# Kernel tuning notes

Measured on AMD Instinct MI355X. Metric: run time of the kernel, lower is better.

## Reference

```python
import jax, jax.numpy as jnp
import numpy as np

B, T, D_MODEL, HEAD = 4, 4096, 1024, 64

def setup_inputs() -> dict:
    key = jax.random.key(0)
    ks = jax.random.split(key, 7)
    s = 0.02  # typical init scale
    return {
        "x":  jax.random.normal(ks[0], (B, T, D_MODEL), dtype=jnp.float32),
        "Wq": jax.random.normal(ks[1], (D_MODEL, HEAD), dtype=jnp.float32) * s,
        "bq": jnp.zeros((HEAD,), dtype=jnp.float32),
        "Wk": jax.random.normal(ks[2], (D_MODEL, HEAD), dtype=jnp.float32) * s,
        "bk": jnp.zeros((HEAD,), dtype=jnp.float32),
        "Wv": jax.random.normal(ks[3], (D_MODEL, HEAD), dtype=jnp.float32) * s,
        "bv": jnp.zeros((HEAD,), dtype=jnp.float32),
    }

def reference(x, Wq, bq, Wk, bk, Wv, bv):
    Bz, Tz, C = x.shape
    q = x @ Wq + bq                      # (B,T,H)
    k = x @ Wk + bk                      # (B,T,H)
    v = x @ Wv + bv                      # (B,T,H)
    # NOTE: original scales by sqrt(C) = sqrt(d_model), not sqrt(head_size)
    att = jnp.einsum("bth,bsh->bts", q, k) / jnp.sqrt(jnp.float32(C))
    causal = jnp.tril(jnp.ones((Tz, Tz), dtype=bool))
    att = jnp.where(causal, att, -jnp.inf)
    att = jax.nn.softmax(att, axis=-1)
    return jnp.einsum("bts,bsh->bth", att, v)  # (B,T,H)
```

## Files before the change

kernel.cpp:

```cpp
#include <hip/hip_runtime.h>
#include <hip/hip_bf16.h>
#include <hip/hip_fp16.h>

#define T_SEQ 4096
#define DMODEL 1024
#define HEAD 64
#define NBATCH 4
#define NSEG 576
#define S2LOG 0.04508422f

typedef __attribute__((ext_vector_type(8))) short bf16x8;
typedef __attribute__((ext_vector_type(4))) float f32x4;

__device__ __forceinline__ unsigned short f2bf(float f) {
    unsigned int b = __float_as_uint(f);
    unsigned int r = b + 0x7FFFu + ((b >> 16) & 1u);
    return (unsigned short)(r >> 16);
}
__device__ __forceinline__ unsigned int pk_bf16(float a, float b) {
    __hip_bfloat162 h = __float22bfloat162_rn(make_float2(a, b));
    unsigned int u; __builtin_memcpy(&u, &h, 4); return u;
}

__global__ __launch_bounds__(256) void prep_w(
    const float* __restrict__ Wq, const float* __restrict__ Wk,
    const float* __restrict__ Wv, unsigned short* __restrict__ Wtb)
{
    __shared__ unsigned short tl[64 * 72];
    const int bid = blockIdx.x;
    const int m   = bid >> 4;
    const int k0  = (bid & 15) * 64;
    const float* W = (m == 0) ? Wq : (m == 1) ? Wk : Wv;
    const int t  = threadIdx.x;
    const int kr = t >> 2, qtr = t & 3;
#pragma unroll
    for (int i = 0; i < 4; ++i) {
        float4 wv4 = *(const float4*)&W[(k0 + kr) * 64 + qtr * 16 + i * 4];
        tl[(qtr * 16 + i * 4 + 0) * 72 + kr] = f2bf(wv4.x);
        tl[(qtr * 16 + i * 4 + 1) * 72 + kr] = f2bf(wv4.y);
        tl[(qtr * 16 + i * 4 + 2) * 72 + kr] = f2bf(wv4.z);
        tl[(qtr * 16 + i * 4 + 3) * 72 + kr] = f2bf(wv4.w);
    }
    __syncthreads();
#pragma unroll
    for (int c = 0; c < 2; ++c) {
        const int lin = c * 256 + t;
        const int n = lin >> 3, k8 = lin & 7;
        *(uint4*)&Wtb[((long)(m * 64 + n)) * 1024 + k0 + k8 * 8] =
            *(const uint4*)&tl[n * 72 + k8 * 8];
    }
}

__global__ __launch_bounds__(256, 2) void qkv_mfma(
    const float* __restrict__ x, const unsigned short* __restrict__ Wtb,
    const float* __restrict__ bq, const float* __restrict__ bk,
    const float* __restrict__ bv,
    unsigned short* __restrict__ qo, unsigned short* __restrict__ ko,
    unsigned short* __restrict__ vt)
{
    __shared__ __align__(16) unsigned short x_s[2][32 * 136];
    const int t    = threadIdx.x;
    const int lane = t & 63;
    const int l15  = lane & 15, quad = lane >> 4;
    const int w    = __builtin_amdgcn_readfirstlane(t >> 6);
    const long row0 = (long)blockIdx.x * 32;

    float bias[3];
#pragma unroll
    for (int ntl = 0; ntl < 3; ++ntl) {
        const int c = w * 48 + ntl * 16 + l15;
        bias[ntl] = (c < 64) ? bq[c] : (c < 128) ? bk[c - 64] : bv[c - 128];
    }
    f32x4 acc[2][3];
#pragma unroll
    for (int mt = 0; mt < 2; ++mt)
#pragma unroll
        for (int ntl = 0; ntl < 3; ++ntl)
            acc[mt][ntl] = (f32x4){bias[ntl], bias[ntl], bias[ntl], bias[ntl]};

    const int srow = t >> 3, sseg = t & 7;
    const float* xp = x + (row0 + srow) * DMODEL + sseg * 16;

    float4 xv[4];
#pragma unroll
    for (int i = 0; i < 4; ++i) xv[i] = *(const float4*)(xp + i * 4);
    {
        unsigned int pk_[8];
#pragma unroll
        for (int i = 0; i < 4; ++i) {
            pk_[i * 2]     = pk_bf16(xv[i].x, xv[i].y);
            pk_[i * 2 + 1] = pk_bf16(xv[i].z, xv[i].w);
        }
        *(uint4*)&x_s[0][srow * 136 + sseg * 16]     = *(const uint4*)&pk_[0];
        *(uint4*)&x_s[0][srow * 136 + sseg * 16 + 8] = *(const uint4*)&pk_[4];
    }
    __syncthreads();

    for (int sg = 0; sg < 8; ++sg) {
        if (sg + 1 < 8)
#pragma unroll
            for (int i = 0; i < 4; ++i)
                xv[i] = *(const float4*)(xp + (sg + 1) * 128 + i * 4);
        bf16x8 wf[3][4];
#pragma unroll
        for (int ntl = 0; ntl < 3; ++ntl)
#pragma unroll
            for (int kq = 0; kq < 4; ++kq)
                wf[ntl][kq] = *(const bf16x8*)&Wtb[((long)(w * 48 + ntl * 16 + l15)) * 1024
                                                   + sg * 128 + kq * 32 + quad * 8];
#pragma unroll
        for (int mt = 0; mt < 2; ++mt)
#pragma unroll
            for (int kq = 0; kq < 4; ++kq) {
                bf16x8 a = *(const bf16x8*)&x_s[sg & 1][(mt * 16 + l15) * 136 + kq * 32 + quad * 8];
#pragma unroll
                for (int ntl = 0; ntl < 3; ++ntl)
                    acc[mt][ntl] = __builtin_amdgcn_mfma_f32_16x16x32_bf16(a, wf[ntl][kq], acc[mt][ntl], 0, 0, 0);
            }
        if (sg + 1 < 8) {
            unsigned int pk_[8];
#pragma unroll
            for (int i = 0; i < 4; ++i) {
                pk_[i * 2]     = pk_bf16(xv[i].x, xv[i].y);
                pk_[i * 2 + 1] = pk_bf16(xv[i].z, xv[i].w);
            }
            *(uint4*)&x_s[(sg + 1) & 1][srow * 136 + sseg * 16]     = *(const uint4*)&pk_[0];
            *(uint4*)&x_s[(sg + 1) & 1][srow * 136 + sseg * 16 + 8] = *(const uint4*)&pk_[4];
        }
        __syncthreads();
    }
#pragma unroll
    for (int mt = 0; mt < 2; ++mt)
#pragma unroll
        for (int ntl = 0; ntl < 3; ++ntl) {
            const int c = w * 48 + ntl * 16 + l15;
            const long tr0 = row0 + mt * 16 + quad * 4;
            if (c < 64) {
#pragma unroll
                for (int r = 0; r < 4; ++r)
                    qo[(tr0 + r) * HEAD + c] = f2bf(acc[mt][ntl][r] * S2LOG);
            } else if (c < 128) {
#pragma unroll
                for (int r = 0; r < 4; ++r)
                    ko[(tr0 + r) * HEAD + (c - 64)] = f2bf(acc[mt][ntl][r]);
            } else {
                const int b = (int)(tr0 >> 12), tloc = (int)(tr0 & 4095);
                uint2 pv;
                pv.x = pk_bf16(acc[mt][ntl][0], acc[mt][ntl][1]);
                pv.y = pk_bf16(acc[mt][ntl][2], acc[mt][ntl][3]);
                *(uint2*)&vt[((long)(b * HEAD + (c - 128))) * T_SEQ + tloc] = pv;
            }
        }
}

__global__ __launch_bounds__(256, 3) void flash_seg(
    const unsigned short* __restrict__ qg,
    const unsigned short* __restrict__ kg,
    const unsigned short* __restrict__ vtg,
    __half* __restrict__ opart, float* __restrict__ ml)
{
    __shared__ __align__(16) unsigned short p_s[4][32 * 72];
    const int t0   = threadIdx.x;
    const int lane = t0 & 63;
    const int l15  = lane & 15, quad = lane >> 4;
    const int wv   = __builtin_amdgcn_readfirstlane(t0 >> 6);

    const int sid = (NSEG - 1) - (int)blockIdx.x;
    int kk = 0, pref = 0;
#pragma unroll
    for (int i = 0; i < 7; ++i) {
        const int cnt = 16 * (kk + 1);
        if (sid >= pref + cnt) { pref += cnt; ++kk; }
    }
    const int S   = kk + 1;
    const int rem = sid - pref;
    const int t   = kk * 16 + rem / S;
    const int si  = rem % S;
    const int r0  = t * 32;
    const int nck = (t + 2) >> 1;
    const int c0  = (si * nck) / S, c1 = ((si + 1) * nck) / S;
    const int b   = wv;
    const long bbase = (long)b * T_SEQ;
    const int gidx = b * NSEG + sid;

    bf16x8 qf[2][2];
#pragma unroll
    for (int s = 0; s < 2; ++s)
#pragma unroll
        for (int h = 0; h < 2; ++h)
            qf[s][h] = *(const bf16x8*)&qg[(bbase + r0 + s * 16 + l15) * HEAD + h * 32 + quad * 8];

    f32x4 o[2][4];
#pragma unroll
    for (int s = 0; s < 2; ++s)
#pragma unroll
        for (int dt = 0; dt < 4; ++dt) o[s][dt] = (f32x4){0.f, 0.f, 0.f, 0.f};
    float mrun[2] = {-30000.f, -30000.f}, lrun[2] = {0.f, 0.f};

    unsigned short* ps = p_s[wv];

    for (int c = c0; c < c1; ++c) {
        const int key0 = c * 64;
        bf16x8 kf[4][2];
#pragma unroll
        for (int mt = 0; mt < 4; ++mt) {
            int krow = key0 + mt * 16 + l15; if (krow > T_SEQ - 1) krow = T_SEQ - 1;
            const unsigned short* kp = &kg[(bbase + krow) * HEAD + quad * 8];
            kf[mt][0] = *(const bf16x8*)kp;
            kf[mt][1] = *(const bf16x8*)(kp + 32);
        }
        f32x4 st[2][4];
#pragma unroll
        for (int s = 0; s < 2; ++s)
#pragma unroll
            for (int mt = 0; mt < 4; ++mt) {
                f32x4 z = (f32x4){0.f, 0.f, 0.f, 0.f};
                z = __builtin_amdgcn_mfma_f32_16x16x32_bf16(kf[mt][0], qf[s][0], z, 0, 0, 0);
                st[s][mt] = __builtin_amdgcn_mfma_f32_16x16x32_bf16(kf[mt][1], qf[s][1], z, 0, 0, 0);
            }
        bf16x8 vf[4][2];
#pragma unroll
        for (int dt = 0; dt < 4; ++dt)
#pragma unroll
            for (int g = 0; g < 2; ++g) {
                int kof = key0 + g * 32 + quad * 8; if (kof > T_SEQ - 8) kof = T_SEQ - 8;
                vf[dt][g] = *(const bf16x8*)&vtg[((long)(b * HEAD + dt * 16 + l15)) * T_SEQ + kof];
            }
        if (key0 + 63 > r0) {
#pragma unroll
            for (int s = 0; s < 2; ++s) {
                const int row = r0 + s * 16 + l15;
#pragma unroll
                for (int mt = 0; mt < 4; ++mt)
#pragma unroll
                    for (int r = 0; r < 4; ++r) {
                        const int key = key0 + mt * 16 + quad * 4 + r;
                        st[s][mt][r] = (key <= row) ? st[s][mt][r] : -30000.f;
                    }
            }
        }
#pragma unroll
        for (int s = 0; s < 2; ++s) {
            float mx = st[s][0][0];
#pragma unroll
            for (int mt = 0; mt < 4; ++mt)
#pragma unroll
                for (int r = 0; r < 4; ++r) mx = fmaxf(mx, st[s][mt][r]);
            mx = fmaxf(mx, __shfl_xor(mx, 16));
            mx = fmaxf(mx, __shfl_xor(mx, 32));
            const float mn = fmaxf(mrun[s], mx);
            const float al = exp2f(mrun[s] - mn);
            mrun[s] = mn;
            float psum = 0.f;
#pragma unroll
            for (int mt = 0; mt < 4; ++mt) {
                float e0 = exp2f(st[s][mt][0] - mn), e1 = exp2f(st[s][mt][1] - mn);
                float e2 = exp2f(st[s][mt][2] - mn), e3 = exp2f(st[s][mt][3] - mn);
                psum += (e0 + e1) + (e2 + e3);
                *(unsigned int*)&ps[(s * 16 + l15) * 72 + mt * 16 + quad * 4]     = pk_bf16(e0, e1);
                *(unsigned int*)&ps[(s * 16 + l15) * 72 + mt * 16 + quad * 4 + 2] = pk_bf16(e2, e3);
            }
            psum += __shfl_xor(psum, 16);
            psum += __shfl_xor(psum, 32);
            lrun[s] = lrun[s] * al + psum;
#pragma unroll
            for (int dt = 0; dt < 4; ++dt)
#pragma unroll
                for (int r = 0; r < 4; ++r) o[s][dt][r] *= al;
        }
        __builtin_amdgcn_wave_barrier();
        bf16x8 pf[2][2];
#pragma unroll
        for (int s = 0; s < 2; ++s)
#pragma unroll
            for (int g = 0; g < 2; ++g)
                pf[s][g] = *(const bf16x8*)&ps[(s * 16 + l15) * 72 + g * 32 + quad * 8];
        __builtin_amdgcn_wave_barrier();
#pragma unroll
        for (int s = 0; s < 2; ++s)
#pragma unroll
            for (int dt = 0; dt < 4; ++dt) {
                o[s][dt] = __builtin_amdgcn_mfma_f32_16x16x32_bf16(vf[dt][0], pf[s][0], o[s][dt], 0, 0, 0);
                o[s][dt] = __builtin_amdgcn_mfma_f32_16x16x32_bf16(vf[dt][1], pf[s][1], o[s][dt], 0, 0, 0);
            }
    }
    __half* op = opart + (long)gidx * 2048;
#pragma unroll
    for (int s = 0; s < 2; ++s) {
#pragma unroll
        for (int dt = 0; dt < 4; ++dt) {
            __half2 h0 = __floats2half2_rn(o[s][dt][0], o[s][dt][1]);
            __half2 h1 = __floats2half2_rn(o[s][dt][2], o[s][dt][3]);
            uint2 u; __builtin_memcpy(&u.x, &h0, 4); __builtin_memcpy(&u.y, &h1, 4);
            *(uint2*)&op[(s * 16 + l15) * HEAD + dt * 16 + quad * 4] = u;
        }
        if (quad == 0) {
            ml[(long)gidx * 64 + s * 16 + l15]      = mrun[s];
            ml[(long)gidx * 64 + 32 + s * 16 + l15] = lrun[s];
        }
    }
}

__global__ __launch_bounds__(256) void merge_seg(
    const __half* __restrict__ opart, const float* __restrict__ ml,
    float* __restrict__ out)
{
    const int bid = blockIdx.x;
    const int t = bid & 127, b = bid >> 7;
    const int kk = t >> 4, S = kk + 1;
    const int base_sid = 8 * kk * (kk + 1) + (t & 15) * S;
    const int tid = threadIdx.x;
    const int row = tid >> 3, col0 = (tid & 7) * 8;

    float m[8], l[8], M = -30000.f;
    for (int si = 0; si < S; ++si) {
        const long g = (long)(b * NSEG + base_sid + si);
        m[si] = ml[g * 64 + row];
        l[si] = ml[g * 64 + 32 + row];
        M = fmaxf(M, m[si]);
    }
    float acc[8];
#pragma unroll
    for (int j = 0; j < 8; ++j) acc[j] = 0.f;
    float L = 0.f;
    for (int si = 0; si < S; ++si) {
        const float wgt = exp2f(m[si] - M);
        L += wgt * l[si];
        const __half* op = opart + (long)(b * NSEG + base_sid + si) * 2048 + row * 64 + col0;
        uint4 u = *(const uint4*)op;
        __half2 h01, h23, h45, h67;
        __builtin_memcpy(&h01, &u.x, 4); __builtin_memcpy(&h23, &u.y, 4);
        __builtin_memcpy(&h45, &u.z, 4); __builtin_memcpy(&h67, &u.w, 4);
        float2 f01 = __half22float2(h01), f23 = __half22float2(h23);
        float2 f45 = __half22float2(h45), f67 = __half22float2(h67);
        acc[0] += wgt * f01.x; acc[1] += wgt * f01.y;
        acc[2] += wgt * f23.x; acc[3] += wgt * f23.y;
        acc[4] += wgt * f45.x; acc[5] += wgt * f45.y;
        acc[6] += wgt * f67.x; acc[7] += wgt * f67.y;
    }
    const float inv = 1.f / L;
    float4 o0 = {acc[0] * inv, acc[1] * inv, acc[2] * inv, acc[3] * inv};
    float4 o1 = {acc[4] * inv, acc[5] * inv, acc[6] * inv, acc[7] * inv};
    float* dst = out + ((long)(b * T_SEQ + t * 32 + row)) * HEAD + col0;
    *(float4*)dst = o0;
    *(float4*)(dst + 4) = o1;
}

extern "C" void kernel_launch(void* const* d_in, const int* in_sizes, int n_in,
                              void* d_out, int out_size, void* d_ws, size_t ws_size,
                              hipStream_t stream) {
    const float* x  = (const float*)d_in[0];
    const float* Wq = (const float*)d_in[1];
    const float* bq = (const float*)d_in[2];
    const float* Wk = (const float*)d_in[3];
    const float* bk = (const float*)d_in[4];
    const float* Wv = (const float*)d_in[5];
    const float* bv = (const float*)d_in[6];
    float* outp = (float*)d_out;

    char* wsb = (char*)d_ws;
    unsigned short* wtb = (unsigned short*)(wsb);
    unsigned short* qw  = (unsigned short*)(wsb + 393216);
    unsigned short* kw  = (unsigned short*)(wsb + 2490368);
    unsigned short* vtw = (unsigned short*)(wsb + 4587520);
    __half* opart       = (__half*)(wsb + 6684672);
    float*  mlp         = (float*)(wsb + 16121856);

    prep_w<<<dim3(48), dim3(256), 0, stream>>>(Wq, Wk, Wv, wtb);
    qkv_mfma<<<dim3(512), dim3(256), 0, stream>>>(
        x, wtb, bq, bk, bv, qw, kw, vtw);
    flash_seg<<<dim3(NSEG), dim3(256), 0, stream>>>(qw, kw, vtw, opart, mlp);
    merge_seg<<<dim3(512), dim3(256), 0, stream>>>(opart, mlp, outp);
}
```

Before: 177.3 us.

## Prefetch K/V double-buffered, split flash blocks per batch, drop LDS staging in QKV

The flash kernel now runs one wave per block, with the batch taken from the block index, and launches four times as many blocks. It double-buffers K and V fragments in registers so the next chunk's loads are issued before the current chunk is processed. The QKV projection kernel drops its shared-memory staging and barriers: each lane reads fp32 x directly from global memory in MFMA fragment layout and converts it to bf16 in registers. The aim is to hide global-load latency and remove barrier overhead, at the cost of more registers and less coalesced x loads.

```diff
diff --git a/kernel.cpp b/kernel.cpp
--- a/kernel.cpp
+++ b/kernel.cpp
@@ -58,7 +58,6 @@
     unsigned short* __restrict__ qo, unsigned short* __restrict__ ko,
     unsigned short* __restrict__ vt)
 {
-    __shared__ __align__(16) unsigned short x_s[2][32 * 136];
     const int t    = threadIdx.x;
     const int lane = t & 63;
     const int l15  = lane & 15, quad = lane >> 4;
@@ -78,56 +77,41 @@
         for (int ntl = 0; ntl < 3; ++ntl)
             acc[mt][ntl] = (f32x4){bias[ntl], bias[ntl], bias[ntl], bias[ntl]};
 
-    const int srow = t >> 3, sseg = t & 7;
-    const float* xp = x + (row0 + srow) * DMODEL + sseg * 16;
-
-    float4 xv[4];
-#pragma unroll
-    for (int i = 0; i < 4; ++i) xv[i] = *(const float4*)(xp + i * 4);
-    {
-        unsigned int pk_[8];
-#pragma unroll
-        for (int i = 0; i < 4; ++i) {
-            pk_[i * 2]     = pk_bf16(xv[i].x, xv[i].y);
-            pk_[i * 2 + 1] = pk_bf16(xv[i].z, xv[i].w);
-        }
-        *(uint4*)&x_s[0][srow * 136 + sseg * 16]     = *(const uint4*)&pk_[0];
-        *(uint4*)&x_s[0][srow * 136 + sseg * 16 + 8] = *(const uint4*)&pk_[4];
-    }
-    __syncthreads();
-
+    const float* xa0 = x + (row0 + l15) * DMODEL + quad * 8;
+    const float* xa1 = x + (row0 + 16 + l15) * DMODEL + quad * 8;
+    const unsigned short* wb = Wtb + ((long)(w * 48 + l15)) * DMODEL + quad * 8;
+
+#pragma unroll 2
     for (int sg = 0; sg < 8; ++sg) {
-        if (sg + 1 < 8)
-#pragma unroll
-            for (int i = 0; i < 4; ++i)
-                xv[i] = *(const float4*)(xp + (sg + 1) * 128 + i * 4);
+        float4 xr[2][4][2];
+#pragma unroll
+        for (int kq = 0; kq < 4; ++kq) {
+            xr[0][kq][0] = *(const float4*)(xa0 + sg * 128 + kq * 32);
+            xr[0][kq][1] = *(const float4*)(xa0 + sg * 128 + kq * 32 + 4);
+            xr[1][kq][0] = *(const float4*)(xa1 + sg * 128 + kq * 32);
+            xr[1][kq][1] = *(const float4*)(xa1 + sg * 128 + kq * 32 + 4);
+        }
         bf16x8 wf[3][4];
 #pragma unroll
         for (int ntl = 0; ntl < 3; ++ntl)
 #pragma unroll
             for (int kq = 0; kq < 4; ++kq)
-                wf[ntl][kq] = *(const bf16x8*)&Wtb[((long)(w * 48 + ntl * 16 + l15)) * 1024
-                                                   + sg * 128 + kq * 32 + quad * 8];
+                wf[ntl][kq] = *(const bf16x8*)(wb + (long)ntl * 16 * DMODEL
+                                               + sg * 128 + kq * 32);
 #pragma unroll
         for (int mt = 0; mt < 2; ++mt)
 #pragma unroll
             for (int kq = 0; kq < 4; ++kq) {
-                bf16x8 a = *(const bf16x8*)&x_s[sg & 1][(mt * 16 + l15) * 136 + kq * 32 + quad * 8];
+                unsigned int u[4];
+                u[0] = pk_bf16(xr[mt][kq][0].x, xr[mt][kq][0].y);
+                u[1] = pk_bf16(xr[mt][kq][0].z, xr[mt][kq][0].w);
+                u[2] = pk_bf16(xr[mt][kq][1].x, xr[mt][kq][1].y);
+                u[3] = pk_bf16(xr[mt][kq][1].z, xr[mt][kq][1].w);
+                bf16x8 a; __builtin_memcpy(&a, u, 16);
 #pragma unroll
                 for (int ntl = 0; ntl < 3; ++ntl)
                     acc[mt][ntl] = __builtin_amdgcn_mfma_f32_16x16x32_bf16(a, wf[ntl][kq], acc[mt][ntl], 0, 0, 0);
             }
-        if (sg + 1 < 8) {
-            unsigned int pk_[8];
-#pragma unroll
-            for (int i = 0; i < 4; ++i) {
-                pk_[i * 2]     = pk_bf16(xv[i].x, xv[i].y);
-                pk_[i * 2 + 1] = pk_bf16(xv[i].z, xv[i].w);
-            }
-            *(uint4*)&x_s[(sg + 1) & 1][srow * 136 + sseg * 16]     = *(const uint4*)&pk_[0];
-            *(uint4*)&x_s[(sg + 1) & 1][srow * 136 + sseg * 16 + 8] = *(const uint4*)&pk_[4];
-        }
-        __syncthreads();
     }
 #pragma unroll
     for (int mt = 0; mt < 2; ++mt)
@@ -153,19 +137,115 @@
         }
 }
 
-__global__ __launch_bounds__(256, 3) void flash_seg(
+struct KV { bf16x8 kf[4][2]; bf16x8 vf[4][2]; };
+
+__device__ __forceinline__ void load_kv(
+    const unsigned short* __restrict__ kg, const unsigned short* __restrict__ vtg,
+    long bbase, int b, int key0, int l15, int quad, KV& r)
+{
+#pragma unroll
+    for (int mt = 0; mt < 4; ++mt) {
+        int krow = key0 + mt * 16 + l15; if (krow > T_SEQ - 1) krow = T_SEQ - 1;
+        const unsigned short* kp = &kg[(bbase + krow) * HEAD + quad * 8];
+        r.kf[mt][0] = *(const bf16x8*)kp;
+        r.kf[mt][1] = *(const bf16x8*)(kp + 32);
+    }
+#pragma unroll
+    for (int dt = 0; dt < 4; ++dt)
+#pragma unroll
+        for (int g = 0; g < 2; ++g) {
+            int kof = key0 + g * 32 + quad * 8; if (kof > T_SEQ - 8) kof = T_SEQ - 8;
+            r.vf[dt][g] = *(const bf16x8*)&vtg[((long)(b * HEAD + dt * 16 + l15)) * T_SEQ + kof];
+        }
+}
+
+__device__ __forceinline__ void process_chunk(
+    int key0, int r0, int l15, int quad,
+    const bf16x8 (&qf)[2][2], const KV& kv, unsigned short* ps,
+    f32x4 (&o)[2][4], float (&mrun)[2], float (&lrun)[2])
+{
+    f32x4 st[2][4];
+#pragma unroll
+    for (int s = 0; s < 2; ++s)
+#pragma unroll
+        for (int mt = 0; mt < 4; ++mt) {
+            f32x4 z = (f32x4){0.f, 0.f, 0.f, 0.f};
+            z = __builtin_amdgcn_mfma_f32_16x16x32_bf16(kv.kf[mt][0], qf[s][0], z, 0, 0, 0);
+            st[s][mt] = __builtin_amdgcn_mfma_f32_16x16x32_bf16(kv.kf[mt][1], qf[s][1], z, 0, 0, 0);
+        }
+    if (key0 + 63 > r0) {
+#pragma unroll
+        for (int s = 0; s < 2; ++s) {
+            const int row = r0 + s * 16 + l15;
+#pragma unroll
+            for (int mt = 0; mt < 4; ++mt)
+#pragma unroll
+                for (int r = 0; r < 4; ++r) {
+                    const int key = key0 + mt * 16 + quad * 4 + r;
+                    st[s][mt][r] = (key <= row) ? st[s][mt][r] : -30000.f;
+                }
+        }
+    }
+#pragma unroll
+    for (int s = 0; s < 2; ++s) {
+        float mx = st[s][0][0];
+#pragma unroll
+        for (int mt = 0; mt < 4; ++mt)
+#pragma unroll
+            for (int r = 0; r < 4; ++r) mx = fmaxf(mx, st[s][mt][r]);
+        mx = fmaxf(mx, __shfl_xor(mx, 16));
+        mx = fmaxf(mx, __shfl_xor(mx, 32));
+        const float mn = fmaxf(mrun[s], mx);
+        const float al = exp2f(mrun[s] - mn);
+        mrun[s] = mn;
+        float psum = 0.f;
+#pragma unroll
+        for (int mt = 0; mt < 4; ++mt) {
+            float e0 = exp2f(st[s][mt][0] - mn), e1 = exp2f(st[s][mt][1] - mn);
+            float e2 = exp2f(st[s][mt][2] - mn), e3 = exp2f(st[s][mt][3] - mn);
+            psum += (e0 + e1) + (e2 + e3);
+            *(unsigned int*)&ps[(s * 16 + l15) * 72 + mt * 16 + quad * 4]     = pk_bf16(e0, e1);
+            *(unsigned int*)&ps[(s * 16 + l15) * 72 + mt * 16 + quad * 4 + 2] = pk_bf16(e2, e3);
+        }
+        psum += __shfl_xor(psum, 16);
+        psum += __shfl_xor(psum, 32);
+        lrun[s] = lrun[s] * al + psum;
+#pragma unroll
+        for (int dt = 0; dt < 4; ++dt)
+#pragma unroll
+            for (int r = 0; r < 4; ++r) o[s][dt][r] *= al;
+    }
+    __builtin_amdgcn_wave_barrier();
+    bf16x8 pf[2][2];
+#pragma unroll
+    for (int s = 0; s < 2; ++s)
+#pragma unroll
+        for (int g = 0; g < 2; ++g)
+            pf[s][g] = *(const bf16x8*)&ps[(s * 16 + l15) * 72 + g * 32 + quad * 8];
+    __builtin_amdgcn_wave_barrier();
+#pragma unroll
+    for (int s = 0; s < 2; ++s)
+#pragma unroll
+        for (int dt = 0; dt < 4; ++dt) {
+            o[s][dt] = __builtin_amdgcn_mfma_f32_16x16x32_bf16(kv.vf[dt][0], pf[s][0], o[s][dt], 0, 0, 0);
+            o[s][dt] = __builtin_amdgcn_mfma_f32_16x16x32_bf16(kv.vf[dt][1], pf[s][1], o[s][dt], 0, 0, 0);
+        }
+}
+
+__global__ __launch_bounds__(64, 2) void flash_seg(
     const unsigned short* __restrict__ qg,
     const unsigned short* __restrict__ kg,
     const unsigned short* __restrict__ vtg,
     __half* __restrict__ opart, float* __restrict__ ml)
 {
-    __shared__ __align__(16) unsigned short p_s[4][32 * 72];
-    const int t0   = threadIdx.x;
-    const int lane = t0 & 63;
+    __shared__ __align__(16) unsigned short p_s[32 * 72];
+    const int lane = threadIdx.x & 63;
     const int l15  = lane & 15, quad = lane >> 4;
-    const int wv   = __builtin_amdgcn_readfirstlane(t0 >> 6);
-
-    const int sid = (NSEG - 1) - (int)blockIdx.x;
+
+    const int bid = (int)blockIdx.x;
+    const int sid = (NSEG - 1) - (bid >> 2);
+    const int b   = bid & 3;
+
     int kk = 0, pref = 0;
 #pragma unroll
     for (int i = 0; i < 7; ++i) {
@@ -179,7 +259,6 @@
     const int r0  = t * 32;
     const int nck = (t + 2) >> 1;
     const int c0  = (si * nck) / S, c1 = ((si + 1) * nck) / S;
-    const int b   = wv;
     const long bbase = (long)b * T_SEQ;
     const int gidx = b * NSEG + sid;
 
@@ -197,93 +276,18 @@
         for (int dt = 0; dt < 4; ++dt) o[s][dt] = (f32x4){0.f, 0.f, 0.f, 0.f};
     float mrun[2] = {-30000.f, -30000.f}, lrun[2] = {0.f, 0.f};
 
-    unsigned short* ps = p_s[wv];
-
+    KV A, B;
+    load_kv(kg, vtg, bbase, b, c0 * 64, l15, quad, A);
     for (int c = c0; c < c1; ++c) {
-        const int key0 = c * 64;
-        bf16x8 kf[4][2];
-#pragma unroll
-        for (int mt = 0; mt < 4; ++mt) {
-            int krow = key0 + mt * 16 + l15; if (krow > T_SEQ - 1) krow = T_SEQ - 1;
-            const unsigned short* kp = &kg[(bbase + krow) * HEAD + quad * 8];
-            kf[mt][0] = *(const bf16x8*)kp;
-            kf[mt][1] = *(const bf16x8*)(kp + 32);
-        }
-        f32x4 st[2][4];
-#pragma unroll
-        for (int s = 0; s < 2; ++s)
-#pragma unroll
-            for (int mt = 0; mt < 4; ++mt) {
-                f32x4 z = (f32x4){0.f, 0.f, 0.f, 0.f};
-                z = __builtin_amdgcn_mfma_f32_16x16x32_bf16(kf[mt][0], qf[s][0], z, 0, 0, 0);
-                st[s][mt] = __builtin_amdgcn_mfma_f32_16x16x32_bf16(kf[mt][1], qf[s][1], z, 0, 0, 0);
-            }
-        bf16x8 vf[4][2];
-#pragma unroll
-        for (int dt = 0; dt < 4; ++dt)
-#pragma unroll
-            for (int g = 0; g < 2; ++g) {
-                int kof = key0 + g * 32 + quad * 8; if (kof > T_SEQ - 8) kof = T_SEQ - 8;
-                vf[dt][g] = *(const bf16x8*)&vtg[((long)(b * HEAD + dt * 16 + l15)) * T_SEQ + kof];
-            }
-        if (key0 + 63 > r0) {
-#pragma unroll
-            for (int s = 0; s < 2; ++s) {
-                const int row = r0 + s * 16 + l15;
-#pragma unroll
-                for (int mt = 0; mt < 4; ++mt)
-#pragma unroll
-                    for (int r = 0; r < 4; ++r) {
-                        const int key = key0 + mt * 16 + quad * 4 + r;
-                        st[s][mt][r] = (key <= row) ? st[s][mt][r] : -30000.f;
-                    }
-            }
-        }
-#pragma unroll
-        for (int s = 0; s < 2; ++s) {
-            float mx = st[s][0][0];
-#pragma unroll
-            for (int mt = 0; mt < 4; ++mt)
-#pragma unroll
-                for (int r = 0; r < 4; ++r) mx = fmaxf(mx, st[s][mt][r]);
-            mx = fmaxf(mx, __shfl_xor(mx, 16));
-            mx = fmaxf(mx, __shfl_xor(mx, 32));
-            const float mn = fmaxf(mrun[s], mx);
-            const float al = exp2f(mrun[s] - mn);
-            mrun[s] = mn;
-            float psum = 0.f;
-#pragma unroll
-            for (int mt = 0; mt < 4; ++mt) {
-                float e0 = exp2f(st[s][mt][0] - mn), e1 = exp2f(st[s][mt][1] - mn);
-                float e2 = exp2f(st[s][mt][2] - mn), e3 = exp2f(st[s][mt][3] - mn);
-                psum += (e0 + e1) + (e2 + e3);
-                *(unsigned int*)&ps[(s * 16 + l15) * 72 + mt * 16 + quad * 4]     = pk_bf16(e0, e1);
-                *(unsigned int*)&ps[(s * 16 + l15) * 72 + mt * 16 + quad * 4 + 2] = pk_bf16(e2, e3);
-            }
-            psum += __shfl_xor(psum, 16);
-            psum += __shfl_xor(psum, 32);
-            lrun[s] = lrun[s] * al + psum;
-#pragma unroll
-            for (int dt = 0; dt < 4; ++dt)
-#pragma unroll
-                for (int r = 0; r < 4; ++r) o[s][dt][r] *= al;
-        }
-        __builtin_amdgcn_wave_barrier();
-        bf16x8 pf[2][2];
-#pragma unroll
-        for (int s = 0; s < 2; ++s)
-#pragma unroll
-            for (int g = 0; g < 2; ++g)
-                pf[s][g] = *(const bf16x8*)&ps[(s * 16 + l15) * 72 + g * 32 + quad * 8];
-        __builtin_amdgcn_wave_barrier();
-#pragma unroll
-        for (int s = 0; s < 2; ++s)
-#pragma unroll
-            for (int dt = 0; dt < 4; ++dt) {
-                o[s][dt] = __builtin_amdgcn_mfma_f32_16x16x32_bf16(vf[dt][0], pf[s][0], o[s][dt], 0, 0, 0);
-                o[s][dt] = __builtin_amdgcn_mfma_f32_16x16x32_bf16(vf[dt][1], pf[s][1], o[s][dt], 0, 0, 0);
-            }
-    }
+        if (((c - c0) & 1) == 0) {
+            if (c + 1 < c1) load_kv(kg, vtg, bbase, b, (c + 1) * 64, l15, quad, B);
+            process_chunk(c * 64, r0, l15, quad, qf, A, p_s, o, mrun, lrun);
+        } else {
+            if (c + 1 < c1) load_kv(kg, vtg, bbase, b, (c + 1) * 64, l15, quad, A);
+            process_chunk(c * 64, r0, l15, quad, qf, B, p_s, o, mrun, lrun);
+        }
+    }
+
     __half* op = opart + (long)gidx * 2048;
 #pragma unroll
     for (int s = 0; s < 2; ++s) {
@@ -369,6 +373,6 @@
     prep_w<<<dim3(48), dim3(256), 0, stream>>>(Wq, Wk, Wv, wtb);
     qkv_mfma<<<dim3(512), dim3(256), 0, stream>>>(
         x, wtb, bq, bk, bv, qw, kw, vtw);
-    flash_seg<<<dim3(NSEG), dim3(256), 0, stream>>>(qw, kw, vtw, opart, mlp);
+    flash_seg<<<dim3(NSEG * NBATCH), dim3(64), 0, stream>>>(qw, kw, vtw, opart, mlp);
     merge_seg<<<dim3(512), dim3(256), 0, stream>>>(opart, mlp, outp);
 }
```

Measured after the change: 261.4 us. 47.4% more time.

## Halve QKV row tile and rebalance flash key-split segments for more blocks

Applied to the files above, without the earlier changes.

The QKV projection kernel now handles 16 rows per block instead of 32 and launches 1024 blocks, giving more parallelism but loading the weight fragments twice as often. The flash attention split-K schedule is redefined so each group of 8 query tiles gets an increasing number of key segments (up to 16), raising segment count from 576 to 1088 for better load balance. The merge kernel and workspace offsets are updated to match. The key/value row clamping is also removed, which saves address math and is safe only if reads never run past the sequence.

```diff
diff --git a/kernel.cpp b/kernel.cpp
--- a/kernel.cpp
+++ b/kernel.cpp
@@ -6,7 +6,7 @@
 #define DMODEL 1024
 #define HEAD 64
 #define NBATCH 4
-#define NSEG 576
+#define NSEG 1088
 #define S2LOG 0.04508422f
 
 typedef __attribute__((ext_vector_type(8))) short bf16x8;
@@ -58,12 +58,12 @@
     unsigned short* __restrict__ qo, unsigned short* __restrict__ ko,
     unsigned short* __restrict__ vt)
 {
-    __shared__ __align__(16) unsigned short x_s[2][32 * 136];
+    __shared__ __align__(16) unsigned short x_s[2][16 * 136];
     const int t    = threadIdx.x;
     const int lane = t & 63;
     const int l15  = lane & 15, quad = lane >> 4;
     const int w    = __builtin_amdgcn_readfirstlane(t >> 6);
-    const long row0 = (long)blockIdx.x * 32;
+    const long row0 = (long)blockIdx.x * 16;
 
     float bias[3];
 #pragma unroll
@@ -71,36 +71,30 @@
         const int c = w * 48 + ntl * 16 + l15;
         bias[ntl] = (c < 64) ? bq[c] : (c < 128) ? bk[c - 64] : bv[c - 128];
     }
-    f32x4 acc[2][3];
-#pragma unroll
-    for (int mt = 0; mt < 2; ++mt)
-#pragma unroll
-        for (int ntl = 0; ntl < 3; ++ntl)
-            acc[mt][ntl] = (f32x4){bias[ntl], bias[ntl], bias[ntl], bias[ntl]};
-
-    const int srow = t >> 3, sseg = t & 7;
-    const float* xp = x + (row0 + srow) * DMODEL + sseg * 16;
-
-    float4 xv[4];
-#pragma unroll
-    for (int i = 0; i < 4; ++i) xv[i] = *(const float4*)(xp + i * 4);
+    f32x4 acc[3];
+#pragma unroll
+    for (int ntl = 0; ntl < 3; ++ntl)
+        acc[ntl] = (f32x4){bias[ntl], bias[ntl], bias[ntl], bias[ntl]};
+
+    const int srow = t >> 4, sseg = t & 15;
+    const float* xp = x + (row0 + srow) * DMODEL + sseg * 8;
+
+    float4 xv[2];
+    xv[0] = *(const float4*)(xp);
+    xv[1] = *(const float4*)(xp + 4);
     {
-        unsigned int pk_[8];
-#pragma unroll
-        for (int i = 0; i < 4; ++i) {
-            pk_[i * 2]     = pk_bf16(xv[i].x, xv[i].y);
-            pk_[i * 2 + 1] = pk_bf16(xv[i].z, xv[i].w);
-        }
-        *(uint4*)&x_s[0][srow * 136 + sseg * 16]     = *(const uint4*)&pk_[0];
-        *(uint4*)&x_s[0][srow * 136 + sseg * 16 + 8] = *(const uint4*)&pk_[4];
+        unsigned int pk_[4];
+        pk_[0] = pk_bf16(xv[0].x, xv[0].y); pk_[1] = pk_bf16(xv[0].z, xv[0].w);
+        pk_[2] = pk_bf16(xv[1].x, xv[1].y); pk_[3] = pk_bf16(xv[1].z, xv[1].w);
+        *(uint4*)&x_s[0][srow * 136 + sseg * 8] = *(const uint4*)&pk_[0];
     }
     __syncthreads();
 
     for (int sg = 0; sg < 8; ++sg) {
-        if (sg + 1 < 8)
-#pragma unroll
-            for (int i = 0; i < 4; ++i)
-                xv[i] = *(const float4*)(xp + (sg + 1) * 128 + i * 4);
+        if (sg + 1 < 8) {
+            xv[0] = *(const float4*)(xp + (sg + 1) * 128);
+            xv[1] = *(const float4*)(xp + (sg + 1) * 128 + 4);
+        }
         bf16x8 wf[3][4];
 #pragma unroll
         for (int ntl = 0; ntl < 3; ++ntl)
@@ -109,48 +103,40 @@
                 wf[ntl][kq] = *(const bf16x8*)&Wtb[((long)(w * 48 + ntl * 16 + l15)) * 1024
                                                    + sg * 128 + kq * 32 + quad * 8];
 #pragma unroll
-        for (int mt = 0; mt < 2; ++mt)
-#pragma unroll
-            for (int kq = 0; kq < 4; ++kq) {
-                bf16x8 a = *(const bf16x8*)&x_s[sg & 1][(mt * 16 + l15) * 136 + kq * 32 + quad * 8];
-#pragma unroll
-                for (int ntl = 0; ntl < 3; ++ntl)
-                    acc[mt][ntl] = __builtin_amdgcn_mfma_f32_16x16x32_bf16(a, wf[ntl][kq], acc[mt][ntl], 0, 0, 0);
-            }
+        for (int kq = 0; kq < 4; ++kq) {
+            bf16x8 a = *(const bf16x8*)&x_s[sg & 1][l15 * 136 + kq * 32 + quad * 8];
+#pragma unroll
+            for (int ntl = 0; ntl < 3; ++ntl)
+                acc[ntl] = __builtin_amdgcn_mfma_f32_16x16x32_bf16(a, wf[ntl][kq], acc[ntl], 0, 0, 0);
+        }
         if (sg + 1 < 8) {
-            unsigned int pk_[8];
-#pragma unroll
-            for (int i = 0; i < 4; ++i) {
-                pk_[i * 2]     = pk_bf16(xv[i].x, xv[i].y);
-                pk_[i * 2 + 1] = pk_bf16(xv[i].z, xv[i].w);
-            }
-            *(uint4*)&x_s[(sg + 1) & 1][srow * 136 + sseg * 16]     = *(const uint4*)&pk_[0];
-            *(uint4*)&x_s[(sg + 1) & 1][srow * 136 + sseg * 16 + 8] = *(const uint4*)&pk_[4];
+            unsigned int pk_[4];
+            pk_[0] = pk_bf16(xv[0].x, xv[0].y); pk_[1] = pk_bf16(xv[0].z, xv[0].w);
+            pk_[2] = pk_bf16(xv[1].x, xv[1].y); pk_[3] = pk_bf16(xv[1].z, xv[1].w);
+            *(uint4*)&x_s[(sg + 1) & 1][srow * 136 + sseg * 8] = *(const uint4*)&pk_[0];
         }
         __syncthreads();
     }
 #pragma unroll
-    for (int mt = 0; mt < 2; ++mt)
-#pragma unroll
-        for (int ntl = 0; ntl < 3; ++ntl) {
-            const int c = w * 48 + ntl * 16 + l15;
-            const long tr0 = row0 + mt * 16 + quad * 4;
-            if (c < 64) {
-#pragma unroll
-                for (int r = 0; r < 4; ++r)
-                    qo[(tr0 + r) * HEAD + c] = f2bf(acc[mt][ntl][r] * S2LOG);
-            } else if (c < 128) {
-#pragma unroll
-                for (int r = 0; r < 4; ++r)
-                    ko[(tr0 + r) * HEAD + (c - 64)] = f2bf(acc[mt][ntl][r]);
-            } else {
-                const int b = (int)(tr0 >> 12), tloc = (int)(tr0 & 4095);
-                uint2 pv;
-                pv.x = pk_bf16(acc[mt][ntl][0], acc[mt][ntl][1]);
-                pv.y = pk_bf16(acc[mt][ntl][2], acc[mt][ntl][3]);
-                *(uint2*)&vt[((long)(b * HEAD + (c - 128))) * T_SEQ + tloc] = pv;
-            }
-        }
+    for (int ntl = 0; ntl < 3; ++ntl) {
+        const int c = w * 48 + ntl * 16 + l15;
+        const long tr0 = row0 + quad * 4;
+        if (c < 64) {
+#pragma unroll
+            for (int r = 0; r < 4; ++r)
+                qo[(tr0 + r) * HEAD + c] = f2bf(acc[ntl][r] * S2LOG);
+        } else if (c < 128) {
+#pragma unroll
+            for (int r = 0; r < 4; ++r)
+                ko[(tr0 + r) * HEAD + (c - 64)] = f2bf(acc[ntl][r]);
+        } else {
+            const int b = (int)(tr0 >> 12), tloc = (int)(tr0 & 4095);
+            uint2 pv;
+            pv.x = pk_bf16(acc[ntl][0], acc[ntl][1]);
+            pv.y = pk_bf16(acc[ntl][2], acc[ntl][3]);
+            *(uint2*)&vt[((long)(b * HEAD + (c - 128))) * T_SEQ + tloc] = pv;
+        }
+    }
 }
 
 __global__ __launch_bounds__(256, 3) void flash_seg(
@@ -168,13 +154,13 @@
     const int sid = (NSEG - 1) - (int)blockIdx.x;
     int kk = 0, pref = 0;
 #pragma unroll
-    for (int i = 0; i < 7; ++i) {
-        const int cnt = 16 * (kk + 1);
+    for (int i = 0; i < 15; ++i) {
+        const int cnt = 8 * (kk + 1);
         if (sid >= pref + cnt) { pref += cnt; ++kk; }
     }
     const int S   = kk + 1;
     const int rem = sid - pref;
-    const int t   = kk * 16 + rem / S;
+    const int t   = kk * 8 + rem / S;
     const int si  = rem % S;
     const int r0  = t * 32;
     const int nck = (t + 2) >> 1;
@@ -204,8 +190,7 @@
         bf16x8 kf[4][2];
 #pragma unroll
         for (int mt = 0; mt < 4; ++mt) {
-            int krow = key0 + mt * 16 + l15; if (krow > T_SEQ - 1) krow = T_SEQ - 1;
-            const unsigned short* kp = &kg[(bbase + krow) * HEAD + quad * 8];
+            const unsigned short* kp = &kg[(bbase + key0 + mt * 16 + l15) * HEAD + quad * 8];
             kf[mt][0] = *(const bf16x8*)kp;
             kf[mt][1] = *(const bf16x8*)(kp + 32);
         }
@@ -222,10 +207,9 @@
 #pragma unroll
         for (int dt = 0; dt < 4; ++dt)
 #pragma unroll
-            for (int g = 0; g < 2; ++g) {
-                int kof = key0 + g * 32 + quad * 8; if (kof > T_SEQ - 8) kof = T_SEQ - 8;
-                vf[dt][g] = *(const bf16x8*)&vtg[((long)(b * HEAD + dt * 16 + l15)) * T_SEQ + kof];
-            }
+            for (int g = 0; g < 2; ++g)
+                vf[dt][g] = *(const bf16x8*)&vtg[((long)(b * HEAD + dt * 16 + l15)) * T_SEQ
+                                                 + key0 + g * 32 + quad * 8];
         if (key0 + 63 > r0) {
 #pragma unroll
             for (int s = 0; s < 2; ++s) {
@@ -284,6 +268,7 @@
                 o[s][dt] = __builtin_amdgcn_mfma_f32_16x16x32_bf16(vf[dt][1], pf[s][1], o[s][dt], 0, 0, 0);
             }
     }
+
     __half* op = opart + (long)gidx * 2048;
 #pragma unroll
     for (int s = 0; s < 2; ++s) {
@@ -307,12 +292,12 @@
 {
     const int bid = blockIdx.x;
     const int t = bid & 127, b = bid >> 7;
-    const int kk = t >> 4, S = kk + 1;
-    const int base_sid = 8 * kk * (kk + 1) + (t & 15) * S;
+    const int kk = t >> 3, S = kk + 1;
+    const int base_sid = 4 * kk * (kk + 1) + (t & 7) * S;
     const int tid = threadIdx.x;
     const int row = tid >> 3, col0 = (tid & 7) * 8;
 
-    float m[8], l[8], M = -30000.f;
+    float m[16], l[16], M = -30000.f;
     for (int si = 0; si < S; ++si) {
         const long g = (long)(b * NSEG + base_sid + si);
         m[si] = ml[g * 64 + row];
@@ -364,10 +349,10 @@
     unsigned short* kw  = (unsigned short*)(wsb + 2490368);
     unsigned short* vtw = (unsigned short*)(wsb + 4587520);
     __half* opart       = (__half*)(wsb + 6684672);
-    float*  mlp         = (float*)(wsb + 16121856);
+    float*  mlp         = (float*)(wsb + 24510464);
 
     prep_w<<<dim3(48), dim3(256), 0, stream>>>(Wq, Wk, Wv, wtb);
-    qkv_mfma<<<dim3(512), dim3(256), 0, stream>>>(
+    qkv_mfma<<<dim3(1024), dim3(256), 0, stream>>>(
         x, wtb, bq, bk, bv, qw, kw, vtw);
     flash_seg<<<dim3(NSEG), dim3(256), 0, stream>>>(qw, kw, vtw, opart, mlp);
     merge_seg<<<dim3(512), dim3(256), 0, stream>>>(opart, mlp, outp);
```

New measurement: 203.1 us. 1.15x slower.

## Split attention into finer key segments and prefetch K and x tiles

Applied to the files above, without the earlier changes.

Regroups flash attention work into 1088 segments, 8 query tiles per group with up to 16 splits, so more blocks share the causal work and the long rows are spread wider. K fragments are double-buffered across key chunks, V loads are issued before the score MFMAs, and the K/V clamps are removed. The QKV projection moves to a three-slot LDS ring with a two-stage register prefetch of x. Occupancy hints drop to 2 for flash_seg, and the merge reads m and l directly instead of staging them in arrays. The tradeoffs are more partial outputs for the merge to combine, extra register pressure, and more workspace.

```diff
diff --git a/kernel.cpp b/kernel.cpp
--- a/kernel.cpp
+++ b/kernel.cpp
@@ -6,7 +6,7 @@
 #define DMODEL 1024
 #define HEAD 64
 #define NBATCH 4
-#define NSEG 576
+#define NSEG 1088
 #define S2LOG 0.04508422f
 
 typedef __attribute__((ext_vector_type(8))) short bf16x8;
@@ -58,7 +58,7 @@
     unsigned short* __restrict__ qo, unsigned short* __restrict__ ko,
     unsigned short* __restrict__ vt)
 {
-    __shared__ __align__(16) unsigned short x_s[2][32 * 136];
+    __shared__ __align__(16) unsigned short x_s[3][32 * 136];
     const int t    = threadIdx.x;
     const int lane = t & 63;
     const int l15  = lane & 15, quad = lane >> 4;
@@ -81,26 +81,30 @@
     const int srow = t >> 3, sseg = t & 7;
     const float* xp = x + (row0 + srow) * DMODEL + sseg * 16;
 
-    float4 xv[4];
-#pragma unroll
-    for (int i = 0; i < 4; ++i) xv[i] = *(const float4*)(xp + i * 4);
+    float4 xv[2][4];
+#pragma unroll
+    for (int i = 0; i < 4; ++i) xv[0][i] = *(const float4*)(xp + i * 4);
     {
         unsigned int pk_[8];
 #pragma unroll
         for (int i = 0; i < 4; ++i) {
-            pk_[i * 2]     = pk_bf16(xv[i].x, xv[i].y);
-            pk_[i * 2 + 1] = pk_bf16(xv[i].z, xv[i].w);
+            pk_[i * 2]     = pk_bf16(xv[0][i].x, xv[0][i].y);
+            pk_[i * 2 + 1] = pk_bf16(xv[0][i].z, xv[0][i].w);
         }
         *(uint4*)&x_s[0][srow * 136 + sseg * 16]     = *(const uint4*)&pk_[0];
         *(uint4*)&x_s[0][srow * 136 + sseg * 16 + 8] = *(const uint4*)&pk_[4];
     }
+#pragma unroll
+    for (int i = 0; i < 4; ++i) xv[1][i] = *(const float4*)(xp + 128 + i * 4);
     __syncthreads();
 
+#pragma unroll
     for (int sg = 0; sg < 8; ++sg) {
-        if (sg + 1 < 8)
+        const int cur = sg % 3;
+        if (sg + 2 < 8)
 #pragma unroll
             for (int i = 0; i < 4; ++i)
-                xv[i] = *(const float4*)(xp + (sg + 1) * 128 + i * 4);
+                xv[sg & 1][i] = *(const float4*)(xp + (sg + 2) * 128 + i * 4);
         bf16x8 wf[3][4];
 #pragma unroll
         for (int ntl = 0; ntl < 3; ++ntl)
@@ -112,7 +116,7 @@
         for (int mt = 0; mt < 2; ++mt)
 #pragma unroll
             for (int kq = 0; kq < 4; ++kq) {
-                bf16x8 a = *(const bf16x8*)&x_s[sg & 1][(mt * 16 + l15) * 136 + kq * 32 + quad * 8];
+                bf16x8 a = *(const bf16x8*)&x_s[cur][(mt * 16 + l15) * 136 + kq * 32 + quad * 8];
 #pragma unroll
                 for (int ntl = 0; ntl < 3; ++ntl)
                     acc[mt][ntl] = __builtin_amdgcn_mfma_f32_16x16x32_bf16(a, wf[ntl][kq], acc[mt][ntl], 0, 0, 0);
@@ -121,11 +125,11 @@
             unsigned int pk_[8];
 #pragma unroll
             for (int i = 0; i < 4; ++i) {
-                pk_[i * 2]     = pk_bf16(xv[i].x, xv[i].y);
-                pk_[i * 2 + 1] = pk_bf16(xv[i].z, xv[i].w);
-            }
-            *(uint4*)&x_s[(sg + 1) & 1][srow * 136 + sseg * 16]     = *(const uint4*)&pk_[0];
-            *(uint4*)&x_s[(sg + 1) & 1][srow * 136 + sseg * 16 + 8] = *(const uint4*)&pk_[4];
+                pk_[i * 2]     = pk_bf16(xv[(sg + 1) & 1][i].x, xv[(sg + 1) & 1][i].y);
+                pk_[i * 2 + 1] = pk_bf16(xv[(sg + 1) & 1][i].z, xv[(sg + 1) & 1][i].w);
+            }
+            *(uint4*)&x_s[(sg + 1) % 3][srow * 136 + sseg * 16]     = *(const uint4*)&pk_[0];
+            *(uint4*)&x_s[(sg + 1) % 3][srow * 136 + sseg * 16 + 8] = *(const uint4*)&pk_[4];
         }
         __syncthreads();
     }
@@ -153,7 +157,7 @@
         }
 }
 
-__global__ __launch_bounds__(256, 3) void flash_seg(
+__global__ __launch_bounds__(256, 2) void flash_seg(
     const unsigned short* __restrict__ qg,
     const unsigned short* __restrict__ kg,
     const unsigned short* __restrict__ vtg,
@@ -168,13 +172,13 @@
     const int sid = (NSEG - 1) - (int)blockIdx.x;
     int kk = 0, pref = 0;
 #pragma unroll
-    for (int i = 0; i < 7; ++i) {
-        const int cnt = 16 * (kk + 1);
+    for (int i = 0; i < 15; ++i) {
+        const int cnt = 8 * (kk + 1);
         if (sid >= pref + cnt) { pref += cnt; ++kk; }
     }
     const int S   = kk + 1;
     const int rem = sid - pref;
-    const int t   = kk * 16 + rem / S;
+    const int t   = kk * 8 + rem / S;
     const int si  = rem % S;
     const int r0  = t * 32;
     const int nck = (t + 2) >> 1;
@@ -199,33 +203,42 @@
 
     unsigned short* ps = p_s[wv];
 
-    for (int c = c0; c < c1; ++c) {
+    bf16x8 kfA[4][2], kfB[4][2];
+    if (c0 < c1) {
+#pragma unroll
+        for (int mt = 0; mt < 4; ++mt) {
+            const unsigned short* kp = &kg[(bbase + c0 * 64 + mt * 16 + l15) * HEAD + quad * 8];
+            kfA[mt][0] = *(const bf16x8*)kp;
+            kfA[mt][1] = *(const bf16x8*)(kp + 32);
+        }
+    }
+
+    auto body = [&](bf16x8 (&kcur)[4][2], bf16x8 (&knxt)[4][2], int c) {
         const int key0 = c * 64;
-        bf16x8 kf[4][2];
-#pragma unroll
-        for (int mt = 0; mt < 4; ++mt) {
-            int krow = key0 + mt * 16 + l15; if (krow > T_SEQ - 1) krow = T_SEQ - 1;
-            const unsigned short* kp = &kg[(bbase + krow) * HEAD + quad * 8];
-            kf[mt][0] = *(const bf16x8*)kp;
-            kf[mt][1] = *(const bf16x8*)(kp + 32);
-        }
+        bf16x8 vf[4][2];
+#pragma unroll
+        for (int dt = 0; dt < 4; ++dt)
+#pragma unroll
+            for (int g = 0; g < 2; ++g)
+                vf[dt][g] = *(const bf16x8*)&vtg[((long)(b * HEAD + dt * 16 + l15)) * T_SEQ
+                                                 + key0 + g * 32 + quad * 8];
         f32x4 st[2][4];
 #pragma unroll
         for (int s = 0; s < 2; ++s)
 #pragma unroll
             for (int mt = 0; mt < 4; ++mt) {
                 f32x4 z = (f32x4){0.f, 0.f, 0.f, 0.f};
-                z = __builtin_amdgcn_mfma_f32_16x16x32_bf16(kf[mt][0], qf[s][0], z, 0, 0, 0);
-                st[s][mt] = __builtin_amdgcn_mfma_f32_16x16x32_bf16(kf[mt][1], qf[s][1], z, 0, 0, 0);
-            }
-        bf16x8 vf[4][2];
-#pragma unroll
-        for (int dt = 0; dt < 4; ++dt)
-#pragma unroll
-            for (int g = 0; g < 2; ++g) {
-                int kof = key0 + g * 32 + quad * 8; if (kof > T_SEQ - 8) kof = T_SEQ - 8;
-                vf[dt][g] = *(const bf16x8*)&vtg[((long)(b * HEAD + dt * 16 + l15)) * T_SEQ + kof];
-            }
+                z = __builtin_amdgcn_mfma_f32_16x16x32_bf16(kcur[mt][0], qf[s][0], z, 0, 0, 0);
+                st[s][mt] = __builtin_amdgcn_mfma_f32_16x16x32_bf16(kcur[mt][1], qf[s][1], z, 0, 0, 0);
+            }
+        if (c + 1 < c1) {
+#pragma unroll
+            for (int mt = 0; mt < 4; ++mt) {
+                const unsigned short* kp = &kg[(bbase + key0 + 64 + mt * 16 + l15) * HEAD + quad * 8];
+                knxt[mt][0] = *(const bf16x8*)kp;
+                knxt[mt][1] = *(const bf16x8*)(kp + 32);
+            }
+        }
         if (key0 + 63 > r0) {
 #pragma unroll
             for (int s = 0; s < 2; ++s) {
@@ -283,7 +296,13 @@
                 o[s][dt] = __builtin_amdgcn_mfma_f32_16x16x32_bf16(vf[dt][0], pf[s][0], o[s][dt], 0, 0, 0);
                 o[s][dt] = __builtin_amdgcn_mfma_f32_16x16x32_bf16(vf[dt][1], pf[s][1], o[s][dt], 0, 0, 0);
             }
-    }
+    };
+
+    for (int c = c0; c < c1; ++c) {
+        if ((c - c0) & 1) body(kfB, kfA, c);
+        else             body(kfA, kfB, c);
+    }
+
     __half* op = opart + (long)gidx * 2048;
 #pragma unroll
     for (int s = 0; s < 2; ++s) {
@@ -307,26 +326,24 @@
 {
     const int bid = blockIdx.x;
     const int t = bid & 127, b = bid >> 7;
-    const int kk = t >> 4, S = kk + 1;
-    const int base_sid = 8 * kk * (kk + 1) + (t & 15) * S;
+    const int kk = t >> 3, S = kk + 1;
+    const int base_sid = 4 * kk * (kk + 1) + (t & 7) * S;
     const int tid = threadIdx.x;
     const int row = tid >> 3, col0 = (tid & 7) * 8;
 
-    float m[8], l[8], M = -30000.f;
-    for (int si = 0; si < S; ++si) {
-        const long g = (long)(b * NSEG + base_sid + si);
-        m[si] = ml[g * 64 + row];
-        l[si] = ml[g * 64 + 32 + row];
-        M = fmaxf(M, m[si]);
-    }
+    float M = -30000.f;
+    for (int si = 0; si < S; ++si)
+        M = fmaxf(M, ml[(long)(b * NSEG + base_sid + si) * 64 + row]);
+
     float acc[8];
 #pragma unroll
     for (int j = 0; j < 8; ++j) acc[j] = 0.f;
     float L = 0.f;
     for (int si = 0; si < S; ++si) {
-        const float wgt = exp2f(m[si] - M);
-        L += wgt * l[si];
-        const __half* op = opart + (long)(b * NSEG + base_sid + si) * 2048 + row * 64 + col0;
+        const long g = (long)(b * NSEG + base_sid + si);
+        const float wgt = exp2f(ml[g * 64 + row] - M);
+        L += wgt * ml[g * 64 + 32 + row];
+        const __half* op = opart + g * 2048 + row * 64 + col0;
         uint4 u = *(const uint4*)op;
         __half2 h01, h23, h45, h67;
         __builtin_memcpy(&h01, &u.x, 4); __builtin_memcpy(&h23, &u.y, 4);
@@ -364,7 +381,7 @@
     unsigned short* kw  = (unsigned short*)(wsb + 2490368);
     unsigned short* vtw = (unsigned short*)(wsb + 4587520);
     __half* opart       = (__half*)(wsb + 6684672);
-    float*  mlp         = (float*)(wsb + 16121856);
+    float*  mlp         = (float*)(wsb + 24510464);
 
     prep_w<<<dim3(48), dim3(256), 0, stream>>>(Wq, Wk, Wv, wtb);
     qkv_mfma<<<dim3(512), dim3(256), 0, stream>>>(
```

Measured after the change: 191.6 us. 8.1% more time.
